# Performance work log

Measured on AMD Instinct MI355X. Metric: run time of the kernel, lower is better.

Reference implementation:

```python
import jax, jax.numpy as jnp
import numpy as np

B, L, D_MODEL, N_HEADS = 4, 2048, 1024, 16
HEAD_DIM = D_MODEL // N_HEADS


def setup_inputs() -> dict:
    key = jax.random.key(0)
    ks = jax.random.split(key, 11)
    s = 1.0 / np.sqrt(D_MODEL)
    return {
        "queries": jax.random.normal(ks[0], (B, L, D_MODEL), jnp.float32),
        "keys": jax.random.normal(ks[1], (B, L, D_MODEL), jnp.float32),
        "values": jax.random.normal(ks[2], (B, L, D_MODEL), jnp.float32),
        "Wq": jax.random.normal(ks[3], (D_MODEL, D_MODEL), jnp.float32) * s,
        "bq": jnp.zeros((D_MODEL,), jnp.float32),
        "Wk": jax.random.normal(ks[4], (D_MODEL, D_MODEL), jnp.float32) * s,
        "bk": jnp.zeros((D_MODEL,), jnp.float32),
        "Wv": jax.random.normal(ks[5], (D_MODEL, D_MODEL), jnp.float32) * s,
        "bv": jnp.zeros((D_MODEL,), jnp.float32),
        "Wo": jax.random.normal(ks[6], (D_MODEL, D_MODEL), jnp.float32) * s,
        "bo": jnp.zeros((D_MODEL,), jnp.float32),
    }


def reference(queries, keys, values, Wq, bq, Wk, bk, Wv, bv, Wo, bo):
    Bsz, Lq, _ = queries.shape
    S = keys.shape[1]
    H, E = N_HEADS, HEAD_DIM
    # QKV projections (weights stored [in, out])
    q = (queries @ Wq + bq).reshape(Bsz, Lq, H, E)
    k = (keys @ Wk + bk).reshape(Bsz, S, H, E)
    v = (values @ Wv + bv).reshape(Bsz, S, H, E)
    scale = 1.0 / np.sqrt(E)
    # scores: [B, H, L, S]
    scores = jnp.einsum("blhe,bshe->bhls", q, k)
    A = jax.nn.softmax(scale * scores, axis=-1)
    # context: [B, L, H, E] -> [B, L, D]
    ctx = jnp.einsum("bhls,bshd->blhd", A, v).reshape(Bsz, Lq, H * E)
    out = ctx @ Wo + bo
    return out
```

## Files before the change

### kernel.cpp

```cpp
#include <hip/hip_runtime.h>

#define BATCH 4
#define SEQ   2048
#define DMODEL 1024
#define NHEADS 16
#define HDIM  64
#define MROWS (BATCH * SEQ)

typedef float f32x4 __attribute__((ext_vector_type(4)));
typedef short s16x8 __attribute__((ext_vector_type(8)));
typedef short s16x4 __attribute__((ext_vector_type(4)));
typedef unsigned short u16;

#define MFMA32K(a, b, c) __builtin_amdgcn_mfma_f32_16x16x32_bf16((a), (b), (c), 0, 0, 0)
#define MFMA16K(a, b, c) __builtin_amdgcn_mfma_f32_16x16x16bf16_1k((a), (b), (c), 0, 0, 0)

__device__ __forceinline__ u16 f2bf(float x) {
    unsigned int u = __builtin_bit_cast(unsigned int, x);
    unsigned int r = u + 0x7fffu + ((u >> 16) & 1u);
    return (u16)(r >> 16);
}

#if __has_builtin(__builtin_amdgcn_cvt_pk_bf16_f32)
__device__ __forceinline__ unsigned int pack2bf(float a, float b) {
    auto r = __builtin_amdgcn_cvt_pk_bf16_f32(a, b);
    return __builtin_bit_cast(unsigned int, r);
}
#else
__device__ __forceinline__ unsigned int pack2bf(float a, float b) {
    return (unsigned int)f2bf(a) | ((unsigned int)f2bf(b) << 16);
}
#endif

__device__ __forceinline__ void dma16(const u16* g, const u16* l) {
    __builtin_amdgcn_global_load_lds(
        (const __attribute__((address_space(1))) unsigned int*)g,
        (__attribute__((address_space(3))) unsigned int*)l, 16, 0, 0);
}
__device__ __forceinline__ void dma16f(const float* g, const float* l) {
    __builtin_amdgcn_global_load_lds(
        (const __attribute__((address_space(1))) unsigned int*)g,
        (__attribute__((address_space(3))) unsigned int*)l, 16, 0, 0);
}

__global__ __launch_bounds__(256) void wconv(const float* __restrict__ W0,
                                             const float* __restrict__ W1,
                                             const float* __restrict__ W2,
                                             const float* __restrict__ W3,
                                             u16* __restrict__ Wt) {
    __shared__ u16 tile[64][80];
    const int t = threadIdx.x;
    const int mtx = blockIdx.z;
    const float* W = (mtx == 0) ? W0 : (mtx == 1) ? W1 : (mtx == 2) ? W2 : W3;
    u16* out = Wt + (size_t)mtx * DMODEL * DMODEL;
    const int n0 = blockIdx.x * 64, k0 = blockIdx.y * 64;
#pragma unroll
    for (int j = 0; j < 4; ++j) {
        int k = j * 16 + (t >> 4);
        int c = (t & 15) * 4;
        float4 v = *(const float4*)(W + (size_t)(k0 + k) * DMODEL + n0 + c);
        tile[c + 0][k] = f2bf(v.x);
        tile[c + 1][k] = f2bf(v.y);
        tile[c + 2][k] = f2bf(v.z);
        tile[c + 3][k] = f2bf(v.w);
    }
    __syncthreads();
#pragma unroll
    for (int i2 = 0; i2 < 2; ++i2) {
        int n = i2 * 32 + (t >> 3), ck = (t & 7) * 8;
        uint4 v = *(const uint4*)(&tile[n][ck]);
        *(uint4*)(out + (size_t)(n0 + n) * DMODEL + k0 + ck) = v;
    }
}

__global__ __launch_bounds__(256) void gemm_qkv(
    const float* __restrict__ Aq, const float* __restrict__ Ak,
    const float* __restrict__ Av, const u16* __restrict__ Wt,
    const float* __restrict__ biq, const float* __restrict__ bik,
    const float* __restrict__ biv, u16* __restrict__ oq, u16* __restrict__ ok,
    u16* __restrict__ ov, float sq) {
    __shared__ float As[128 * 32];
    __shared__ u16 Bs[128 * 32];
    const int t = threadIdx.x;
    const int w = t >> 6, lane = t & 63, quad = lane >> 4, l16 = lane & 15;
    const int z = blockIdx.z;
    const float* A = (z == 0) ? Aq : (z == 1) ? Ak : Av;
    const u16* B = Wt + (size_t)z * DMODEL * DMODEL;
    const float* bias = (z == 0) ? biq : (z == 1) ? bik : biv;
    u16* C = (z == 0) ? oq : (z == 1) ? ok : ov;
    const float scale = (z == 0) ? sq : 1.0f;
    const int n0 = blockIdx.x * 128, m0 = blockIdx.y * 128;
    const int wm = (w >> 1) * 64, wn = (w & 1) * 64;

    f32x4 acc[4][4] = {};

    const int arow = (lane >> 3);
    const int aunit = (lane & 7) ^ (2 * (arow & 3));
    const int brow = (lane >> 2);
    const int bcol = (lane & 3) * 8;

    for (int k0 = 0; k0 < DMODEL; k0 += 32) {
#pragma unroll
        for (int j = 0; j < 4; ++j) {
            int row = w * 32 + j * 8 + arow;
            dma16f(A + (size_t)(m0 + row) * DMODEL + k0 + aunit * 4,
                   &As[(w * 32 + j * 8) * 32]);
        }
#pragma unroll
        for (int j = 0; j < 2; ++j) {
            int row = w * 32 + j * 16 + brow;
            dma16(B + (size_t)(n0 + row) * DMODEL + k0 + bcol,
                  &Bs[(w * 32 + j * 16) * 32]);
        }
        __syncthreads();

        s16x8 af[4], bf[4];
#pragma unroll
        for (int mt = 0; mt < 4; ++mt) {
            int row = wm + mt * 16 + l16;
            int u0 = 2 * (quad ^ (l16 & 3));
            const float* pa = &As[row * 32 + u0 * 4];
            f32x4 lo = *(const f32x4*)pa;
            f32x4 hi = *(const f32x4*)(pa + 4);
            uint4 pk_;
            pk_.x = pack2bf(lo[0], lo[1]);
            pk_.y = pack2bf(lo[2], lo[3]);
            pk_.z = pack2bf(hi[0], hi[1]);
            pk_.w = pack2bf(hi[2], hi[3]);
            af[mt] = __builtin_bit_cast(s16x8, pk_);
        }
#pragma unroll
        for (int nt = 0; nt < 4; ++nt)
            bf[nt] = *(const s16x8*)(&Bs[(wn + nt * 16 + l16) * 32 + quad * 8]);
#pragma unroll
        for (int mt = 0; mt < 4; ++mt)
#pragma unroll
            for (int nt = 0; nt < 4; ++nt)
                acc[mt][nt] = MFMA32K(af[mt], bf[nt], acc[mt][nt]);
        __syncthreads();
    }

#pragma unroll
    for (int mt = 0; mt < 4; ++mt)
#pragma unroll
        for (int nt = 0; nt < 4; ++nt) {
            int col = n0 + wn + nt * 16 + l16;
            float bv_ = bias[col];
#pragma unroll
            for (int r = 0; r < 4; ++r) {
                int row = m0 + wm + mt * 16 + quad * 4 + r;
                C[(size_t)row * DMODEL + col] = f2bf((acc[mt][nt][r] + bv_) * scale);
            }
        }
}

__global__ __launch_bounds__(256) void gemm_o(const u16* __restrict__ A,
                                              const u16* __restrict__ Bt,
                                              const float* __restrict__ bias,
                                              float* __restrict__ Cp) {
    __shared__ u16 As[128 * 32];
    __shared__ u16 Bs[128 * 32];
    const int t = threadIdx.x;
    const int w = t >> 6, lane = t & 63, quad = lane >> 4, l16 = lane & 15;
    const int n0 = blockIdx.x * 128, m0 = blockIdx.y * 128;
    const int wm = (w >> 1) * 64, wn = (w & 1) * 64;
    const int lr = lane >> 2, lc = (lane & 3) * 8;

    f32x4 acc[4][4] = {};

    for (int k0 = 0; k0 < DMODEL; k0 += 32) {
#pragma unroll
        for (int j = 0; j < 2; ++j) {
            int row = w * 32 + j * 16;
            dma16(A + (size_t)(m0 + row + lr) * DMODEL + k0 + lc, &As[row * 32]);
            dma16(Bt + (size_t)(n0 + row + lr) * DMODEL + k0 + lc, &Bs[row * 32]);
        }
        __syncthreads();
        s16x8 af[4], bf[4];
#pragma unroll
        for (int mt = 0; mt < 4; ++mt)
            af[mt] = *(const s16x8*)(&As[(wm + mt * 16 + l16) * 32 + quad * 8]);
#pragma unroll
        for (int nt = 0; nt < 4; ++nt)
            bf[nt] = *(const s16x8*)(&Bs[(wn + nt * 16 + l16) * 32 + quad * 8]);
#pragma unroll
        for (int mt = 0; mt < 4; ++mt)
#pragma unroll
            for (int nt = 0; nt < 4; ++nt)
                acc[mt][nt] = MFMA32K(af[mt], bf[nt], acc[mt][nt]);
        __syncthreads();
    }

#pragma unroll
    for (int mt = 0; mt < 4; ++mt)
#pragma unroll
        for (int nt = 0; nt < 4; ++nt) {
            int col = n0 + wn + nt * 16 + l16;
            float bv_ = bias[col];
#pragma unroll
            for (int r = 0; r < 4; ++r) {
                int row = m0 + wm + mt * 16 + quad * 4 + r;
                Cp[(size_t)row * DMODEL + col] = acc[mt][nt][r] + bv_;
            }
        }
}

__global__ __launch_bounds__(256) void attn3(const u16* __restrict__ qb,
                                             const u16* __restrict__ kb,
                                             const u16* __restrict__ vb,
                                             u16* __restrict__ ctxb) {
    __shared__ u16 Ks[64 * 64];
    __shared__ u16 Vt[64 * 72];
    const int t = threadIdx.x;
    const int w = t >> 6, lane = t & 63, quad = lane >> 4, l16 = lane & 15;
    const int b = blockIdx.z, h = blockIdx.y, q0 = blockIdx.x * 128;

    s16x8 bq[2][2];
#pragma unroll
    for (int qs = 0; qs < 2; ++qs) {
        size_t base = (size_t)(b * SEQ + q0 + w * 32 + qs * 16 + l16) * DMODEL + h * HDIM + quad * 8;
        bq[qs][0] = *(const s16x8*)(qb + base);
        bq[qs][1] = *(const s16x8*)(qb + base + 32);
    }

    const int krow = lane >> 3;
    const int kunit = (lane & 7) ^ (krow & 7);

    float lsum[2] = {0.0f, 0.0f};
    f32x4 o[2][4] = {};

    for (int s0 = 0; s0 < SEQ; s0 += 64) {
        __syncthreads();
#pragma unroll
        for (int j = 0; j < 2; ++j) {
            int row = w * 16 + j * 8 + krow;
            dma16(kb + (size_t)(b * SEQ + s0 + row) * DMODEL + h * HDIM + kunit * 8,
                  &Ks[(w * 16 + j * 8) * 64]);
        }
#pragma unroll
        for (int i = 0; i < 2; ++i) {
            int idx = i * 256 + t;
            int key = idx >> 3, seg = idx & 7;
            union { uint4 v; u16 s[8]; } u;
            u.v = *(const uint4*)(vb + (size_t)(b * SEQ + s0 + key) * DMODEL + h * HDIM + seg * 8);
            int col = (((key >> 3) ^ seg) << 3) + (key & 7);
#pragma unroll
            for (int ii = 0; ii < 8; ++ii)
                Vt[(seg * 8 + ii) * 72 + col] = u.s[ii];
        }
        __syncthreads();

        s16x8 ak[4][2];
#pragma unroll
        for (int kt = 0; kt < 4; ++kt) {
            int row = kt * 16 + l16;
#pragma unroll
            for (int hf = 0; hf < 2; ++hf) {
                int un = (hf * 4 + quad) ^ (l16 & 7);
                ak[kt][hf] = *(const s16x8*)(&Ks[row * 64 + un * 8]);
            }
        }

        unsigned int pk[2][4][2];
#pragma unroll
        for (int qs = 0; qs < 2; ++qs) {
            f32x4 sc[4];
#pragma unroll
            for (int kt = 0; kt < 4; ++kt) {
                f32x4 zz = {0.0f, 0.0f, 0.0f, 0.0f};
                zz = MFMA32K(ak[kt][0], bq[qs][0], zz);
                sc[kt] = MFMA32K(ak[kt][1], bq[qs][1], zz);
            }
            float rs = 0.0f;
            float p[4][4];
#pragma unroll
            for (int kt = 0; kt < 4; ++kt)
#pragma unroll
                for (int r = 0; r < 4; ++r) {
                    p[kt][r] = __builtin_amdgcn_exp2f(sc[kt][r]);
                    rs += p[kt][r];
                }
            rs += __shfl_xor(rs, 16);
            rs += __shfl_xor(rs, 32);
            lsum[qs] += rs;
#pragma unroll
            for (int kt = 0; kt < 4; ++kt) {
                pk[qs][kt][0] = pack2bf(p[kt][0], p[kt][1]);
                pk[qs][kt][1] = pack2bf(p[kt][2], p[kt][3]);
            }
        }

#pragma unroll
        for (int mt = 0; mt < 4; ++mt) {
            const int dim = mt * 16 + l16;
            const int swz = (dim >> 3) & 7;
            const int rowoff = dim * 72;
#pragma unroll
            for (int kt = 0; kt < 4; ++kt) {
                int col = ((((kt * 2) + (quad >> 1)) ^ swz) << 3) + ((quad & 1) << 2);
                s16x4 av = *(const s16x4*)(&Vt[rowoff + col]);
#pragma unroll
                for (int qs = 0; qs < 2; ++qs) {
                    union { unsigned int u[2]; s16x4 v; } pb;
                    pb.u[0] = pk[qs][kt][0];
                    pb.u[1] = pk[qs][kt][1];
                    o[qs][mt] = MFMA16K(av, pb.v, o[qs][mt]);
                }
            }
        }
    }

#pragma unroll
    for (int qs = 0; qs < 2; ++qs) {
        float rl = 1.0f / lsum[qs];
        size_t rowbase = (size_t)(b * SEQ + q0 + w * 32 + qs * 16 + l16) * DMODEL + h * HDIM;
#pragma unroll
        for (int mt = 0; mt < 4; ++mt)
#pragma unroll
            for (int rr = 0; rr < 2; ++rr) {
                unsigned int v = pack2bf(o[qs][mt][rr * 2] * rl, o[qs][mt][rr * 2 + 1] * rl);
                *(unsigned int*)(&ctxb[rowbase + mt * 16 + quad * 4 + rr * 2]) = v;
            }
    }
}

extern "C" void kernel_launch(void* const* d_in, const int* in_sizes, int n_in,
                              void* d_out, int out_size, void* d_ws, size_t ws_size,
                              hipStream_t stream) {
    const float* queries = (const float*)d_in[0];
    const float* keys    = (const float*)d_in[1];
    const float* values  = (const float*)d_in[2];
    const float* Wq = (const float*)d_in[3];
    const float* bq = (const float*)d_in[4];
    const float* Wk = (const float*)d_in[5];
    const float* bk = (const float*)d_in[6];
    const float* Wv = (const float*)d_in[7];
    const float* bv = (const float*)d_in[8];
    const float* Wo = (const float*)d_in[9];
    const float* bo = (const float*)d_in[10];
    float* out = (float*)d_out;

    char* ws = (char*)d_ws;
    u16* Wt   = (u16*)ws;
    u16* qbuf = (u16*)(ws + ((size_t)8 << 20));
    u16* kbuf = (u16*)(ws + ((size_t)24 << 20));
    u16* vbuf = (u16*)(ws + ((size_t)40 << 20));
    u16* ctxb = qbuf;

    const size_t WSZ = (size_t)DMODEL * DMODEL;
    const float S2 = 0.125f * 1.44269504088896340736f;

    dim3 blk(256);

    wconv<<<dim3(16, 16, 4), blk, 0, stream>>>(Wq, Wk, Wv, Wo, Wt);

    gemm_qkv<<<dim3(8, 64, 3), blk, 0, stream>>>(queries, keys, values, Wt,
                                                 bq, bk, bv, qbuf, kbuf, vbuf, S2);

    attn3<<<dim3(SEQ / 128, NHEADS, BATCH), blk, 0, stream>>>(qbuf, kbuf, vbuf, ctxb);

    gemm_o<<<dim3(8, 64), blk, 0, stream>>>(ctxb, Wt + 3 * WSZ, bo, out);
}
```

Baseline: 424.2 us.

## Pre-convert activations to bf16 and reorder grid so M varies fastest

New measurement: 377.5 us. 11.0% less time.

```diff
diff --git a/kernel.cpp b/kernel.cpp
--- a/kernel.cpp
+++ b/kernel.cpp
@@ -37,10 +37,21 @@
         (const __attribute__((address_space(1))) unsigned int*)g,
         (__attribute__((address_space(3))) unsigned int*)l, 16, 0, 0);
 }
-__device__ __forceinline__ void dma16f(const float* g, const float* l) {
-    __builtin_amdgcn_global_load_lds(
-        (const __attribute__((address_space(1))) unsigned int*)g,
-        (__attribute__((address_space(3))) unsigned int*)l, 16, 0, 0);
+
+__global__ __launch_bounds__(256) void convk3(
+    const float* __restrict__ s0, const float* __restrict__ s1,
+    const float* __restrict__ s2, u16* __restrict__ d0, u16* __restrict__ d1,
+    u16* __restrict__ d2) {
+    const int z = blockIdx.y;
+    const float* src = (z == 0) ? s0 : (z == 1) ? s1 : s2;
+    u16* dst = (z == 0) ? d0 : (z == 1) ? d1 : d2;
+    const int i = blockIdx.x * 256 + threadIdx.x;
+    float4 a = ((const float4*)src)[i * 2];
+    float4 b = ((const float4*)src)[i * 2 + 1];
+    uint4 o;
+    o.x = pack2bf(a.x, a.y); o.y = pack2bf(a.z, a.w);
+    o.z = pack2bf(b.x, b.y); o.w = pack2bf(b.z, b.w);
+    *(uint4*)(dst + (size_t)i * 8) = o;
 }
 
 __global__ __launch_bounds__(256) void wconv(const float* __restrict__ W0,
@@ -74,61 +85,39 @@
 }
 
 __global__ __launch_bounds__(256) void gemm_qkv(
-    const float* __restrict__ Aq, const float* __restrict__ Ak,
-    const float* __restrict__ Av, const u16* __restrict__ Wt,
+    const u16* __restrict__ Aq, const u16* __restrict__ Ak,
+    const u16* __restrict__ Av, const u16* __restrict__ Wt,
     const float* __restrict__ biq, const float* __restrict__ bik,
     const float* __restrict__ biv, u16* __restrict__ oq, u16* __restrict__ ok,
     u16* __restrict__ ov, float sq) {
-    __shared__ float As[128 * 32];
+    __shared__ u16 As[128 * 32];
     __shared__ u16 Bs[128 * 32];
     const int t = threadIdx.x;
     const int w = t >> 6, lane = t & 63, quad = lane >> 4, l16 = lane & 15;
     const int z = blockIdx.z;
-    const float* A = (z == 0) ? Aq : (z == 1) ? Ak : Av;
+    const u16* A = (z == 0) ? Aq : (z == 1) ? Ak : Av;
     const u16* B = Wt + (size_t)z * DMODEL * DMODEL;
     const float* bias = (z == 0) ? biq : (z == 1) ? bik : biv;
     u16* C = (z == 0) ? oq : (z == 1) ? ok : ov;
     const float scale = (z == 0) ? sq : 1.0f;
-    const int n0 = blockIdx.x * 128, m0 = blockIdx.y * 128;
+    const int m0 = blockIdx.x * 128, n0 = blockIdx.y * 128;
     const int wm = (w >> 1) * 64, wn = (w & 1) * 64;
+    const int lr = lane >> 2, lc = (lane & 3) * 8;
 
     f32x4 acc[4][4] = {};
 
-    const int arow = (lane >> 3);
-    const int aunit = (lane & 7) ^ (2 * (arow & 3));
-    const int brow = (lane >> 2);
-    const int bcol = (lane & 3) * 8;
-
     for (int k0 = 0; k0 < DMODEL; k0 += 32) {
 #pragma unroll
-        for (int j = 0; j < 4; ++j) {
-            int row = w * 32 + j * 8 + arow;
-            dma16f(A + (size_t)(m0 + row) * DMODEL + k0 + aunit * 4,
-                   &As[(w * 32 + j * 8) * 32]);
-        }
-#pragma unroll
         for (int j = 0; j < 2; ++j) {
-            int row = w * 32 + j * 16 + brow;
-            dma16(B + (size_t)(n0 + row) * DMODEL + k0 + bcol,
-                  &Bs[(w * 32 + j * 16) * 32]);
-        }
-        __syncthreads();
-
+            int row = w * 32 + j * 16;
+            dma16(A + (size_t)(m0 + row + lr) * DMODEL + k0 + lc, &As[row * 32]);
+            dma16(B + (size_t)(n0 + row + lr) * DMODEL + k0 + lc, &Bs[row * 32]);
+        }
+        __syncthreads();
         s16x8 af[4], bf[4];
 #pragma unroll
-        for (int mt = 0; mt < 4; ++mt) {
-            int row = wm + mt * 16 + l16;
-            int u0 = 2 * (quad ^ (l16 & 3));
-            const float* pa = &As[row * 32 + u0 * 4];
-            f32x4 lo = *(const f32x4*)pa;
-            f32x4 hi = *(const f32x4*)(pa + 4);
-            uint4 pk_;
-            pk_.x = pack2bf(lo[0], lo[1]);
-            pk_.y = pack2bf(lo[2], lo[3]);
-            pk_.z = pack2bf(hi[0], hi[1]);
-            pk_.w = pack2bf(hi[2], hi[3]);
-            af[mt] = __builtin_bit_cast(s16x8, pk_);
-        }
+        for (int mt = 0; mt < 4; ++mt)
+            af[mt] = *(const s16x8*)(&As[(wm + mt * 16 + l16) * 32 + quad * 8]);
 #pragma unroll
         for (int nt = 0; nt < 4; ++nt)
             bf[nt] = *(const s16x8*)(&Bs[(wn + nt * 16 + l16) * 32 + quad * 8]);
@@ -162,7 +151,7 @@
     __shared__ u16 Bs[128 * 32];
     const int t = threadIdx.x;
     const int w = t >> 6, lane = t & 63, quad = lane >> 4, l16 = lane & 15;
-    const int n0 = blockIdx.x * 128, m0 = blockIdx.y * 128;
+    const int m0 = blockIdx.x * 128, n0 = blockIdx.y * 128;
     const int wm = (w >> 1) * 64, wn = (w & 1) * 64;
     const int lr = lane >> 2, lc = (lane & 3) * 8;
 
@@ -213,7 +202,7 @@
     __shared__ u16 Vt[64 * 72];
     const int t = threadIdx.x;
     const int w = t >> 6, lane = t & 63, quad = lane >> 4, l16 = lane & 15;
-    const int b = blockIdx.z, h = blockIdx.y, q0 = blockIdx.x * 128;
+    const int h = blockIdx.x, b = blockIdx.z, q0 = blockIdx.y * 128;
 
     s16x8 bq[2][2];
 #pragma unroll
@@ -342,9 +331,12 @@
 
     char* ws = (char*)d_ws;
     u16* Wt   = (u16*)ws;
-    u16* qbuf = (u16*)(ws + ((size_t)8 << 20));
-    u16* kbuf = (u16*)(ws + ((size_t)24 << 20));
-    u16* vbuf = (u16*)(ws + ((size_t)40 << 20));
+    u16* aq   = (u16*)(ws + ((size_t)8 << 20));
+    u16* ak   = (u16*)(ws + ((size_t)24 << 20));
+    u16* av   = (u16*)(ws + ((size_t)40 << 20));
+    u16* qbuf = (u16*)(ws + ((size_t)56 << 20));
+    u16* kbuf = (u16*)(ws + ((size_t)72 << 20));
+    u16* vbuf = (u16*)(ws + ((size_t)88 << 20));
     u16* ctxb = qbuf;
 
     const size_t WSZ = (size_t)DMODEL * DMODEL;
@@ -353,11 +345,12 @@
     dim3 blk(256);
 
     wconv<<<dim3(16, 16, 4), blk, 0, stream>>>(Wq, Wk, Wv, Wo, Wt);
-
-    gemm_qkv<<<dim3(8, 64, 3), blk, 0, stream>>>(queries, keys, values, Wt,
+    convk3<<<dim3(4096, 3), blk, 0, stream>>>(queries, keys, values, aq, ak, av);
+
+    gemm_qkv<<<dim3(64, 8, 3), blk, 0, stream>>>(aq, ak, av, Wt,
                                                  bq, bk, bv, qbuf, kbuf, vbuf, S2);
 
-    attn3<<<dim3(SEQ / 128, NHEADS, BATCH), blk, 0, stream>>>(qbuf, kbuf, vbuf, ctxb);
-
-    gemm_o<<<dim3(8, 64), blk, 0, stream>>>(ctxb, Wt + 3 * WSZ, bo, out);
-}
+    attn3<<<dim3(NHEADS, SEQ / 128, BATCH), blk, 0, stream>>>(qbuf, kbuf, vbuf, ctxb);
+
+    gemm_o<<<dim3(64, 8), blk, 0, stream>>>(ctxb, Wt + 3 * WSZ, bo, out);
+}
```
